# Optimization experiments

Measured on AMD Instinct MI355X. Metric: run time of the kernel, lower is better.

The kernel has to match this reference:

```python
import jax, jax.numpy as jnp
import numpy as np

NUM_HEADS = 16
WINDOW = 256  # window_size; tokens attend iff |i-j| <= WINDOW//2
LN_EPS = 1e-5


def setup_inputs() -> dict:
    key = jax.random.key(0)
    k1, k2, k3 = jax.random.split(key, 3)
    B, L, D = 2, 2048, 1024
    x = jax.random.normal(k1, (B, L, D), dtype=jnp.float32)
    w_qkv = jax.random.normal(k2, (3 * D, D), dtype=jnp.float32) * 0.02
    w_out = jax.random.normal(k3, (D, D), dtype=jnp.float32) * 0.02
    gamma = jnp.ones((D,), dtype=jnp.float32)
    beta = jnp.zeros((D,), dtype=jnp.float32)
    return {"x": x, "w_qkv": w_qkv, "w_out": w_out, "gamma": gamma, "beta": beta}


def reference(x, w_qkv, w_out, gamma, beta):
    B, L, D = x.shape
    H = NUM_HEADS
    HD = D // H
    residual = x
    # LayerNorm
    mu = jnp.mean(x, axis=-1, keepdims=True)
    var = jnp.mean(jnp.square(x - mu), axis=-1, keepdims=True)
    xn = (x - mu) * jax.lax.rsqrt(var + LN_EPS) * gamma + beta
    # QKV projection (torch Linear: y = x @ W.T)
    qkv = jnp.einsum('bld,ed->ble', xn, w_qkv).reshape(B, L, 3, H, HD)
    qkv = jnp.transpose(qkv, (2, 0, 3, 1, 4))  # [3, B, H, L, HD]
    q, k, v = qkv[0], qkv[1], qkv[2]
    # Dense scores with banded window mask (same math as the torch module)
    scores = jnp.einsum('bhqd,bhkd->bhqk', q, k) / jnp.sqrt(jnp.float32(HD))
    idx = jnp.arange(L)
    band = jnp.abs(idx[:, None] - idx[None, :]) <= (WINDOW // 2)  # [L, L] bool
    scores = jnp.where(band[None, None], scores, -jnp.inf)
    attn = jax.nn.softmax(scores, axis=-1)
    out = jnp.einsum('bhqk,bhkd->bhqd', attn, v)  # [B, H, L, HD]
    out = jnp.transpose(out, (0, 2, 1, 3)).reshape(B, L, D)
    return residual + jnp.einsum('bld,ed->ble', out, w_out)
```

## Files before the change

kernel.cpp:

```cpp
#include <hip/hip_runtime.h>

typedef unsigned int u32;
typedef unsigned short u16;
typedef __attribute__((ext_vector_type(8))) short short8;
typedef __attribute__((ext_vector_type(4))) float f32x4;

#define LSEQ 2048
#define DM 1024
#define HWIN 128

__device__ __forceinline__ u16 f2bf(float f) {
  union { float f; u32 u; } v; v.f = f;
  u32 r = v.u + 0x7FFFu + ((v.u >> 16) & 1u);
  return (u16)(r >> 16);
}
__device__ __forceinline__ u32 packbf(float lo, float hi) {
  return (u32)f2bf(lo) | ((u32)f2bf(hi) << 16);
}

typedef __attribute__((address_space(3))) u32 lds_u32;
typedef __attribute__((address_space(1))) const u32 glob_u32;
__device__ __forceinline__ void g2lds16(const void* g, void* l) {
  __builtin_amdgcn_global_load_lds((glob_u32*)g, (lds_u32*)l, 16, 0, 0);
}

__global__ __launch_bounds__(256) void ln_kernel(const float* __restrict__ x,
                                                 const float* __restrict__ gamma,
                                                 const float* __restrict__ beta,
                                                 u16* __restrict__ xn) {
  int r = blockIdx.x;
  int t = threadIdx.x;
  const float4* xr = (const float4*)(x + (size_t)r * DM);
  float4 v = xr[t];
  float s = v.x + v.y + v.z + v.w;
  float s2 = v.x * v.x + v.y * v.y + v.z * v.z + v.w * v.w;
#pragma unroll
  for (int o = 32; o; o >>= 1) { s += __shfl_xor(s, o); s2 += __shfl_xor(s2, o); }
  __shared__ float ws1[4], ws2[4];
  if ((t & 63) == 0) { ws1[t >> 6] = s; ws2[t >> 6] = s2; }
  __syncthreads();
  s = ws1[0] + ws1[1] + ws1[2] + ws1[3];
  s2 = ws2[0] + ws2[1] + ws2[2] + ws2[3];
  float mu = s * (1.0f / DM);
  float var = s2 * (1.0f / DM) - mu * mu;
  float rs = rsqrtf(var + 1e-5f);
  float4 g = ((const float4*)gamma)[t];
  float4 b = ((const float4*)beta)[t];
  u32 lo = packbf((v.x - mu) * rs * g.x + b.x, (v.y - mu) * rs * g.y + b.y);
  u32 hi = packbf((v.z - mu) * rs * g.z + b.z, (v.w - mu) * rs * g.w + b.w);
  u32* dst = (u32*)(xn + (size_t)r * DM) + t * 2;
  dst[0] = lo; dst[1] = hi;
}

__global__ __launch_bounds__(256) void cvt2_kernel(const float* __restrict__ a,
                                                   const float* __restrict__ b,
                                                   u16* __restrict__ oa,
                                                   u16* __restrict__ ob) {
  int blk = blockIdx.x;
  const float* in; u16* out; int i;
  if (blk < 3072) { in = a; out = oa; i = blk * 256 + threadIdx.x; }
  else            { in = b; out = ob; i = (blk - 3072) * 256 + threadIdx.x; }
  float4 v = ((const float4*)in)[i];
  u32* dst = (u32*)out + i * 2;
  dst[0] = packbf(v.x, v.y);
  dst[1] = packbf(v.z, v.w);
}

__device__ __forceinline__ void stage_tile(const u16* __restrict__ G, int gr0, int K,
                                           int k0, u16* lbuf, int tid, int w) {
#pragma unroll
  for (int j = 0; j < 4; ++j) {
    int rp = j * 32 + (tid >> 3);
    int ce = ((tid & 7) ^ (rp & 7)) * 8;
    g2lds16(G + (size_t)(gr0 + rp) * K + k0 + ce, lbuf + j * 2048 + w * 512);
  }
}

template <int MODE>
__global__ __launch_bounds__(256) void gemm_bt(const u16* __restrict__ Ag,
                                               const u16* __restrict__ Bg,
                                               int K, int NB,
                                               u16* __restrict__ qk_out,
                                               u16* __restrict__ vt_out,
                                               const float* __restrict__ resid,
                                               float* __restrict__ out) {
  __shared__ __align__(16) u16 sm[32768];
  int tid = threadIdx.x;
  int w = tid >> 6, l = tid & 63;
  int lg = l >> 4, li = l & 15;
  int bm = blockIdx.x / NB, bn = blockIdx.x % NB;
  int wr = w >> 1, wc = w & 1;
  f32x4 acc[4][4];
#pragma unroll
  for (int m = 0; m < 4; ++m)
#pragma unroll
    for (int n = 0; n < 4; ++n) acc[m][n] = (f32x4){0.f, 0.f, 0.f, 0.f};

  int nt = K >> 6;
  stage_tile(Ag, bm * 128, K, 0, sm, tid, w);
  stage_tile(Bg, bn * 128, K, 0, sm + 8192, tid, w);
  asm volatile("s_waitcnt vmcnt(0)" ::: "memory");
  __builtin_amdgcn_s_barrier();
  asm volatile("" ::: "memory");

  int cur = 0;
  for (int t = 0; t < nt; ++t) {
    if (t + 1 < nt) {
      stage_tile(Ag, bm * 128, K, (t + 1) << 6, sm + (cur ^ 1) * 16384, tid, w);
      stage_tile(Bg, bn * 128, K, (t + 1) << 6, sm + (cur ^ 1) * 16384 + 8192, tid, w);
    }
    const u16* Ab = sm + cur * 16384;
    const u16* Bb = Ab + 8192;
#pragma unroll
    for (int ks = 0; ks < 2; ++ks) {
      short8 af[4], bf4[4];
#pragma unroll
      for (int m = 0; m < 4; ++m)
        af[m] = *(const short8*)&Ab[(wr * 64 + m * 16 + li) * 64 + (((lg + ks * 4) ^ (li & 7)) * 8)];
#pragma unroll
      for (int n = 0; n < 4; ++n)
        bf4[n] = *(const short8*)&Bb[(wc * 64 + n * 16 + li) * 64 + (((lg + ks * 4) ^ (li & 7)) * 8)];
#pragma unroll
      for (int m = 0; m < 4; ++m)
#pragma unroll
        for (int n = 0; n < 4; ++n)
          acc[m][n] = __builtin_amdgcn_mfma_f32_16x16x32_bf16(af[m], bf4[n], acc[m][n], 0, 0, 0);
    }
    asm volatile("s_waitcnt vmcnt(0)" ::: "memory");
    __builtin_amdgcn_s_barrier();
    asm volatile("" ::: "memory");
    cur ^= 1;
  }

  int colbase = bn * 128 + wc * 64;
  int rowbase = bm * 128 + wr * 64;
#pragma unroll
  for (int m = 0; m < 4; ++m) {
    int row = rowbase + m * 16 + lg * 4;
#pragma unroll
    for (int n = 0; n < 4; ++n) {
      int col = colbase + n * 16 + li;
      if (MODE == 0) {
        if (colbase < 2048) {
#pragma unroll
          for (int r = 0; r < 4; ++r)
            qk_out[(size_t)(row + r) * 2048 + col] = f2bf(acc[m][n][r]);
        } else {
          int b = row >> 11;
          int hdcol = col - 2048;
          size_t idx = ((size_t)b * 1024 + hdcol) * 2048 + (row & 2047);
          u32* d = (u32*)&vt_out[idx];
          d[0] = packbf(acc[m][n][0], acc[m][n][1]);
          d[1] = packbf(acc[m][n][2], acc[m][n][3]);
        }
      } else {
#pragma unroll
        for (int r = 0; r < 4; ++r) {
          size_t idx = (size_t)(row + r) * 1024 + col;
          out[idx] = resid[idx] + acc[m][n][r];
        }
      }
    }
  }
}

__global__ __launch_bounds__(256) void attn_kernel(const u16* __restrict__ qk,
                                                   const u16* __restrict__ vt,
                                                   u16* __restrict__ ato) {
  int blk = blockIdx.x;
  int bh = blk >> 5;
  int qblk = blk & 31;
  int b = bh >> 4, h = bh & 15;
  int tid = threadIdx.x;
  int w = tid >> 6, l = tid & 63;
  int lg = l >> 4, li = l & 15;
  int qw = qblk * 64 + w * 16;
  int q = qw + li;

  const u16* qbase = qk + (size_t)(b * 2048 + q) * 2048 + h * 64 + lg * 8;
  short8 qf0 = *(const short8*)qbase;
  short8 qf1 = *(const short8*)(qbase + 32);

  const u16* kbase = qk + (size_t)b * 2048 * 2048 + 1024 + h * 64 + lg * 8;
  const u16* vbase = vt + (size_t)(bh * 64 + li) * 2048;

  f32x4 o0 = {0,0,0,0}, o1 = {0,0,0,0}, o2 = {0,0,0,0}, o3 = {0,0,0,0};
  float m = -1e30f, lsum = 0.f;

  int lo = qw - HWIN; if (lo < 0) lo = 0;
  int hi = qw + 15 + HWIN; if (hi > LSEQ - 1) hi = LSEQ - 1;
  const float SC = 0.125f * 1.44269504088896f;

  for (int kb = lo & ~31; kb <= hi; kb += 32) {
    const u16* kp0 = kbase + (size_t)(kb + li) * 2048;
    const u16* kp1 = kbase + (size_t)(kb + 16 + li) * 2048;
    short8 k00 = *(const short8*)kp0;
    short8 k01 = *(const short8*)(kp0 + 32);
    short8 k10 = *(const short8*)kp1;
    short8 k11 = *(const short8*)(kp1 + 32);
    f32x4 c0 = {0,0,0,0}, c1 = {0,0,0,0};
    c0 = __builtin_amdgcn_mfma_f32_16x16x32_bf16(k00, qf0, c0, 0, 0, 0);
    c0 = __builtin_amdgcn_mfma_f32_16x16x32_bf16(k01, qf1, c0, 0, 0, 0);
    c1 = __builtin_amdgcn_mfma_f32_16x16x32_bf16(k10, qf0, c1, 0, 0, 0);
    c1 = __builtin_amdgcn_mfma_f32_16x16x32_bf16(k11, qf1, c1, 0, 0, 0);

    float t[8];
    bool interior = (kb >= qw + 15 - HWIN) && (kb + 31 <= qw + HWIN) && (kb + 31 < LSEQ);
    if (interior) {
#pragma unroll
      for (int r = 0; r < 4; ++r) { t[r] = c0[r] * SC; t[r + 4] = c1[r] * SC; }
    } else {
#pragma unroll
      for (int r = 0; r < 4; ++r) {
        int key0 = kb + lg * 4 + r;
        int key1 = key0 + 16;
        int d0 = key0 - q, d1 = key1 - q;
        t[r]     = (d0 >= -HWIN && d0 <= HWIN && key0 < LSEQ) ? c0[r] * SC : -__builtin_inff();
        t[r + 4] = (d1 >= -HWIN && d1 <= HWIN && key1 < LSEQ) ? c1[r] * SC : -__builtin_inff();
      }
    }
    float mc = t[0];
#pragma unroll
    for (int i = 1; i < 8; ++i) mc = fmaxf(mc, t[i]);
    mc = fmaxf(mc, __shfl_xor(mc, 16));
    mc = fmaxf(mc, __shfl_xor(mc, 32));

    float p[8]; float ssum;
    if (__all(mc <= m + 8.0f)) {
      ssum = 0.f;
#pragma unroll
      for (int i = 0; i < 8; ++i) { p[i] = __builtin_amdgcn_exp2f(t[i] - m); ssum += p[i]; }
      ssum += __shfl_xor(ssum, 16);
      ssum += __shfl_xor(ssum, 32);
      lsum += ssum;
    } else {
      float mn = fmaxf(m, mc);
      float corr = __builtin_amdgcn_exp2f(m - mn);
      ssum = 0.f;
#pragma unroll
      for (int i = 0; i < 8; ++i) { p[i] = __builtin_amdgcn_exp2f(t[i] - mn); ssum += p[i]; }
      ssum += __shfl_xor(ssum, 16);
      ssum += __shfl_xor(ssum, 32);
      lsum = lsum * corr + ssum;
      m = mn;
      o0 *= corr; o1 *= corr; o2 *= corr; o3 *= corr;
    }

    u32 a0 = packbf(p[0], p[1]);
    u32 a1 = packbf(p[2], p[3]);
    u32 b0 = packbf(p[4], p[5]);
    u32 b1 = packbf(p[6], p[7]);
    int sg0 = (((2 * lg) & 3) << 4) + li;
    int sg1 = (((2 * lg + 1) & 3) << 4) + li;
    u32 w0 = (u32)__shfl((int)a0, sg0), w1 = (u32)__shfl((int)a1, sg0);
    u32 w2 = (u32)__shfl((int)a0, sg1), w3 = (u32)__shfl((int)a1, sg1);
    u32 x0 = (u32)__shfl((int)b0, sg0), x1 = (u32)__shfl((int)b1, sg0);
    u32 x2 = (u32)__shfl((int)b0, sg1), x3 = (u32)__shfl((int)b1, sg1);
    bool lohalf = lg < 2;
    union { u32 u[4]; short8 s; } pf;
    pf.u[0] = lohalf ? w0 : x0;
    pf.u[1] = lohalf ? w1 : x1;
    pf.u[2] = lohalf ? w2 : x2;
    pf.u[3] = lohalf ? w3 : x3;

    const u16* vp = vbase + kb + lg * 8;
    short8 v0 = *(const short8*)(vp);
    short8 v1 = *(const short8*)(vp + (size_t)16 * 2048);
    short8 v2 = *(const short8*)(vp + (size_t)32 * 2048);
    short8 v3 = *(const short8*)(vp + (size_t)48 * 2048);
    o0 = __builtin_amdgcn_mfma_f32_16x16x32_bf16(v0, pf.s, o0, 0, 0, 0);
    o1 = __builtin_amdgcn_mfma_f32_16x16x32_bf16(v1, pf.s, o1, 0, 0, 0);
    o2 = __builtin_amdgcn_mfma_f32_16x16x32_bf16(v2, pf.s, o2, 0, 0, 0);
    o3 = __builtin_amdgcn_mfma_f32_16x16x32_bf16(v3, pf.s, o3, 0, 0, 0);
  }

  float inv = 1.0f / lsum;
  u16* orow = ato + (size_t)(b * 2048 + q) * 1024 + h * 64 + lg * 4;
  *(u32*)(orow +  0) = packbf(o0[0] * inv, o0[1] * inv);
  *(u32*)(orow +  2) = packbf(o0[2] * inv, o0[3] * inv);
  *(u32*)(orow + 16) = packbf(o1[0] * inv, o1[1] * inv);
  *(u32*)(orow + 18) = packbf(o1[2] * inv, o1[3] * inv);
  *(u32*)(orow + 32) = packbf(o2[0] * inv, o2[1] * inv);
  *(u32*)(orow + 34) = packbf(o2[2] * inv, o2[3] * inv);
  *(u32*)(orow + 48) = packbf(o3[0] * inv, o3[1] * inv);
  *(u32*)(orow + 50) = packbf(o3[2] * inv, o3[3] * inv);
}

extern "C" void kernel_launch(void* const* d_in, const int* in_sizes, int n_in,
                              void* d_out, int out_size, void* d_ws, size_t ws_size,
                              hipStream_t stream) {
  const float* x     = (const float*)d_in[0];
  const float* w_qkv = (const float*)d_in[1];
  const float* w_out = (const float*)d_in[2];
  const float* gamma = (const float*)d_in[3];
  const float* beta  = (const float*)d_in[4];
  float* out = (float*)d_out;
  char* ws = (char*)d_ws;

  u16* xn  = (u16*)(ws);
  u16* wq  = (u16*)(ws + 8388608);
  u16* wo  = (u16*)(ws + 14680064);
  u16* qkb = (u16*)(ws + 16777216);
  u16* vt  = (u16*)(ws + 33554432);
  u16* ao  = (u16*)(ws + 41943040);

  ln_kernel<<<4096, 256, 0, stream>>>(x, gamma, beta, xn);
  cvt2_kernel<<<4096, 256, 0, stream>>>(w_qkv, w_out, wq, wo);
  gemm_bt<0><<<32 * 24, 256, 0, stream>>>(xn, wq, 1024, 24, qkb, vt, nullptr, nullptr);
  attn_kernel<<<32 * 32, 256, 0, stream>>>(qkb, vt, ao);
  gemm_bt<1><<<32 * 8, 256, 0, stream>>>(ao, wo, 1024, 8, nullptr, nullptr, x, out);
}
```

Baseline: 105.8 us.

## Software-pipeline K/V loads in attention and merge LN with weight conversion

The attention loop now double-buffers K and V register fragments, issuing the next chunk's global loads before computing the current one. The per-chunk cross-lane row-sum reduction is deferred to a single reduction after the loop, and the redundant sequence-end checks are dropped. Launch bounds request 4 blocks per SM. Separately, the LayerNorm and weight bf16 conversion kernels are merged into one launch to cut one kernel launch. The double-buffered fragments raise register pressure, which may reduce occupancy.

```diff
diff --git a/kernel.cpp b/kernel.cpp
--- a/kernel.cpp
+++ b/kernel.cpp
@@ -24,12 +24,27 @@
   __builtin_amdgcn_global_load_lds((glob_u32*)g, (lds_u32*)l, 16, 0, 0);
 }
 
-__global__ __launch_bounds__(256) void ln_kernel(const float* __restrict__ x,
-                                                 const float* __restrict__ gamma,
-                                                 const float* __restrict__ beta,
-                                                 u16* __restrict__ xn) {
-  int r = blockIdx.x;
+__global__ __launch_bounds__(256) void ln_cvt_kernel(const float* __restrict__ x,
+                                                     const float* __restrict__ gamma,
+                                                     const float* __restrict__ beta,
+                                                     u16* __restrict__ xn,
+                                                     const float* __restrict__ wqi,
+                                                     const float* __restrict__ woi,
+                                                     u16* __restrict__ wq,
+                                                     u16* __restrict__ wo) {
+  int blk = blockIdx.x;
   int t = threadIdx.x;
+  if (blk >= 4096) {
+    const float* in; u16* out; int i;
+    if (blk < 7168) { in = wqi; out = wq; i = (blk - 4096) * 256 + t; }
+    else            { in = woi; out = wo; i = (blk - 7168) * 256 + t; }
+    float4 v = ((const float4*)in)[i];
+    u32* dst = (u32*)out + i * 2;
+    dst[0] = packbf(v.x, v.y);
+    dst[1] = packbf(v.z, v.w);
+    return;
+  }
+  int r = blk;
   const float4* xr = (const float4*)(x + (size_t)r * DM);
   float4 v = xr[t];
   float s = v.x + v.y + v.z + v.w;
@@ -52,20 +67,6 @@
   dst[0] = lo; dst[1] = hi;
 }
 
-__global__ __launch_bounds__(256) void cvt2_kernel(const float* __restrict__ a,
-                                                   const float* __restrict__ b,
-                                                   u16* __restrict__ oa,
-                                                   u16* __restrict__ ob) {
-  int blk = blockIdx.x;
-  const float* in; u16* out; int i;
-  if (blk < 3072) { in = a; out = oa; i = blk * 256 + threadIdx.x; }
-  else            { in = b; out = ob; i = (blk - 3072) * 256 + threadIdx.x; }
-  float4 v = ((const float4*)in)[i];
-  u32* dst = (u32*)out + i * 2;
-  dst[0] = packbf(v.x, v.y);
-  dst[1] = packbf(v.z, v.w);
-}
-
 __device__ __forceinline__ void stage_tile(const u16* __restrict__ G, int gr0, int K,
                                            int k0, u16* lbuf, int tid, int w) {
 #pragma unroll
@@ -164,9 +165,100 @@
   }
 }
 
-__global__ __launch_bounds__(256) void attn_kernel(const u16* __restrict__ qk,
-                                                   const u16* __restrict__ vt,
-                                                   u16* __restrict__ ato) {
+__device__ __forceinline__ void process_chunk(
+    short8 k00, short8 k01, short8 k10, short8 k11,
+    short8 v0, short8 v1, short8 v2, short8 v3,
+    short8 qf0, short8 qf1,
+    int kb, int qw, int q, int lg, int sg0, int sg1,
+    float& mrun, float& lsum, f32x4& o0, f32x4& o1, f32x4& o2, f32x4& o3) {
+  const float SC = 0.125f * 1.44269504088896f;
+  f32x4 c0 = {0,0,0,0}, c1 = {0,0,0,0};
+  c0 = __builtin_amdgcn_mfma_f32_16x16x32_bf16(k00, qf0, c0, 0, 0, 0);
+  c0 = __builtin_amdgcn_mfma_f32_16x16x32_bf16(k01, qf1, c0, 0, 0, 0);
+  c1 = __builtin_amdgcn_mfma_f32_16x16x32_bf16(k10, qf0, c1, 0, 0, 0);
+  c1 = __builtin_amdgcn_mfma_f32_16x16x32_bf16(k11, qf1, c1, 0, 0, 0);
+
+  float t[8];
+  bool interior = (kb >= qw + 15 - HWIN) && (kb + 31 <= qw + HWIN);
+  if (interior) {
+#pragma unroll
+    for (int r = 0; r < 4; ++r) { t[r] = c0[r] * SC; t[r + 4] = c1[r] * SC; }
+  } else {
+#pragma unroll
+    for (int r = 0; r < 4; ++r) {
+      int key0 = kb + lg * 4 + r;
+      int key1 = key0 + 16;
+      int d0 = key0 - q, d1 = key1 - q;
+      t[r]     = (d0 >= -HWIN && d0 <= HWIN) ? c0[r] * SC : -__builtin_inff();
+      t[r + 4] = (d1 >= -HWIN && d1 <= HWIN) ? c1[r] * SC : -__builtin_inff();
+    }
+  }
+  float mA = fmaxf(fmaxf(t[0], t[1]), fmaxf(t[2], t[3]));
+  float mB = fmaxf(fmaxf(t[4], t[5]), fmaxf(t[6], t[7]));
+  float mc = fmaxf(mA, mB);
+  mc = fmaxf(mc, __shfl_xor(mc, 16));
+  mc = fmaxf(mc, __shfl_xor(mc, 32));
+
+  float p[8];
+  if (__all(mc <= mrun + 8.0f)) {
+    float s0 = 0.f;
+#pragma unroll
+    for (int i = 0; i < 8; ++i) { p[i] = __builtin_amdgcn_exp2f(t[i] - mrun); s0 += p[i]; }
+    lsum += s0;
+  } else {
+    float mn = fmaxf(mrun, mc);
+    float corr = __builtin_amdgcn_exp2f(mrun - mn);
+    float s0 = 0.f;
+#pragma unroll
+    for (int i = 0; i < 8; ++i) { p[i] = __builtin_amdgcn_exp2f(t[i] - mn); s0 += p[i]; }
+    lsum = lsum * corr + s0;
+    mrun = mn;
+    o0 *= corr; o1 *= corr; o2 *= corr; o3 *= corr;
+  }
+
+  u32 a0 = packbf(p[0], p[1]);
+  u32 a1 = packbf(p[2], p[3]);
+  u32 b0 = packbf(p[4], p[5]);
+  u32 b1 = packbf(p[6], p[7]);
+  u32 w0 = (u32)__shfl((int)a0, sg0), w1 = (u32)__shfl((int)a1, sg0);
+  u32 w2 = (u32)__shfl((int)a0, sg1), w3 = (u32)__shfl((int)a1, sg1);
+  u32 x0 = (u32)__shfl((int)b0, sg0), x1 = (u32)__shfl((int)b1, sg0);
+  u32 x2 = (u32)__shfl((int)b0, sg1), x3 = (u32)__shfl((int)b1, sg1);
+  bool lohalf = lg < 2;
+  union { u32 u[4]; short8 s; } pf;
+  pf.u[0] = lohalf ? w0 : x0;
+  pf.u[1] = lohalf ? w1 : x1;
+  pf.u[2] = lohalf ? w2 : x2;
+  pf.u[3] = lohalf ? w3 : x3;
+
+  o0 = __builtin_amdgcn_mfma_f32_16x16x32_bf16(v0, pf.s, o0, 0, 0, 0);
+  o1 = __builtin_amdgcn_mfma_f32_16x16x32_bf16(v1, pf.s, o1, 0, 0, 0);
+  o2 = __builtin_amdgcn_mfma_f32_16x16x32_bf16(v2, pf.s, o2, 0, 0, 0);
+  o3 = __builtin_amdgcn_mfma_f32_16x16x32_bf16(v3, pf.s, o3, 0, 0, 0);
+}
+
+#define LOADKV(P, kb)                                                        \
+  do {                                                                       \
+    const u16* kp0_ = kbase + (size_t)((kb) + li) * 2048;                    \
+    const u16* kp1_ = kp0_ + (size_t)16 * 2048;                              \
+    P##k00 = *(const short8*)kp0_;                                           \
+    P##k01 = *(const short8*)(kp0_ + 32);                                    \
+    P##k10 = *(const short8*)kp1_;                                           \
+    P##k11 = *(const short8*)(kp1_ + 32);                                    \
+    const u16* vp_ = vbase + (kb) + lg * 8;                                  \
+    P##v0 = *(const short8*)vp_;                                             \
+    P##v1 = *(const short8*)(vp_ + (size_t)16 * 2048);                       \
+    P##v2 = *(const short8*)(vp_ + (size_t)32 * 2048);                       \
+    P##v3 = *(const short8*)(vp_ + (size_t)48 * 2048);                       \
+  } while (0)
+
+#define PROC(P, kb)                                                          \
+  process_chunk(P##k00, P##k01, P##k10, P##k11, P##v0, P##v1, P##v2, P##v3,  \
+                qf0, qf1, (kb), qw, q, lg, sg0, sg1, mrun, lsum, o0, o1, o2, o3)
+
+__global__ __launch_bounds__(256, 4) void attn_kernel(const u16* __restrict__ qk,
+                                                      const u16* __restrict__ vt,
+                                                      u16* __restrict__ ato) {
   int blk = blockIdx.x;
   int bh = blk >> 5;
   int qblk = blk & 31;
@@ -176,6 +268,8 @@
   int lg = l >> 4, li = l & 15;
   int qw = qblk * 64 + w * 16;
   int q = qw + li;
+  int sg0 = (((2 * lg) & 3) << 4) + li;
+  int sg1 = (((2 * lg + 1) & 3) << 4) + li;
 
   const u16* qbase = qk + (size_t)(b * 2048 + q) * 2048 + h * 64 + lg * 8;
   short8 qf0 = *(const short8*)qbase;
@@ -185,95 +279,29 @@
   const u16* vbase = vt + (size_t)(bh * 64 + li) * 2048;
 
   f32x4 o0 = {0,0,0,0}, o1 = {0,0,0,0}, o2 = {0,0,0,0}, o3 = {0,0,0,0};
-  float m = -1e30f, lsum = 0.f;
+  float mrun = -1e30f, lsum = 0.f;
 
   int lo = qw - HWIN; if (lo < 0) lo = 0;
   int hi = qw + 15 + HWIN; if (hi > LSEQ - 1) hi = LSEQ - 1;
-  const float SC = 0.125f * 1.44269504088896f;
-
-  for (int kb = lo & ~31; kb <= hi; kb += 32) {
-    const u16* kp0 = kbase + (size_t)(kb + li) * 2048;
-    const u16* kp1 = kbase + (size_t)(kb + 16 + li) * 2048;
-    short8 k00 = *(const short8*)kp0;
-    short8 k01 = *(const short8*)(kp0 + 32);
-    short8 k10 = *(const short8*)kp1;
-    short8 k11 = *(const short8*)(kp1 + 32);
-    f32x4 c0 = {0,0,0,0}, c1 = {0,0,0,0};
-    c0 = __builtin_amdgcn_mfma_f32_16x16x32_bf16(k00, qf0, c0, 0, 0, 0);
-    c0 = __builtin_amdgcn_mfma_f32_16x16x32_bf16(k01, qf1, c0, 0, 0, 0);
-    c1 = __builtin_amdgcn_mfma_f32_16x16x32_bf16(k10, qf0, c1, 0, 0, 0);
-    c1 = __builtin_amdgcn_mfma_f32_16x16x32_bf16(k11, qf1, c1, 0, 0, 0);
-
-    float t[8];
-    bool interior = (kb >= qw + 15 - HWIN) && (kb + 31 <= qw + HWIN) && (kb + 31 < LSEQ);
-    if (interior) {
-#pragma unroll
-      for (int r = 0; r < 4; ++r) { t[r] = c0[r] * SC; t[r + 4] = c1[r] * SC; }
-    } else {
-#pragma unroll
-      for (int r = 0; r < 4; ++r) {
-        int key0 = kb + lg * 4 + r;
-        int key1 = key0 + 16;
-        int d0 = key0 - q, d1 = key1 - q;
-        t[r]     = (d0 >= -HWIN && d0 <= HWIN && key0 < LSEQ) ? c0[r] * SC : -__builtin_inff();
-        t[r + 4] = (d1 >= -HWIN && d1 <= HWIN && key1 < LSEQ) ? c1[r] * SC : -__builtin_inff();
-      }
-    }
-    float mc = t[0];
-#pragma unroll
-    for (int i = 1; i < 8; ++i) mc = fmaxf(mc, t[i]);
-    mc = fmaxf(mc, __shfl_xor(mc, 16));
-    mc = fmaxf(mc, __shfl_xor(mc, 32));
-
-    float p[8]; float ssum;
-    if (__all(mc <= m + 8.0f)) {
-      ssum = 0.f;
-#pragma unroll
-      for (int i = 0; i < 8; ++i) { p[i] = __builtin_amdgcn_exp2f(t[i] - m); ssum += p[i]; }
-      ssum += __shfl_xor(ssum, 16);
-      ssum += __shfl_xor(ssum, 32);
-      lsum += ssum;
-    } else {
-      float mn = fmaxf(m, mc);
-      float corr = __builtin_amdgcn_exp2f(m - mn);
-      ssum = 0.f;
-#pragma unroll
-      for (int i = 0; i < 8; ++i) { p[i] = __builtin_amdgcn_exp2f(t[i] - mn); ssum += p[i]; }
-      ssum += __shfl_xor(ssum, 16);
-      ssum += __shfl_xor(ssum, 32);
-      lsum = lsum * corr + ssum;
-      m = mn;
-      o0 *= corr; o1 *= corr; o2 *= corr; o3 *= corr;
-    }
-
-    u32 a0 = packbf(p[0], p[1]);
-    u32 a1 = packbf(p[2], p[3]);
-    u32 b0 = packbf(p[4], p[5]);
-    u32 b1 = packbf(p[6], p[7]);
-    int sg0 = (((2 * lg) & 3) << 4) + li;
-    int sg1 = (((2 * lg + 1) & 3) << 4) + li;
-    u32 w0 = (u32)__shfl((int)a0, sg0), w1 = (u32)__shfl((int)a1, sg0);
-    u32 w2 = (u32)__shfl((int)a0, sg1), w3 = (u32)__shfl((int)a1, sg1);
-    u32 x0 = (u32)__shfl((int)b0, sg0), x1 = (u32)__shfl((int)b1, sg0);
-    u32 x2 = (u32)__shfl((int)b0, sg1), x3 = (u32)__shfl((int)b1, sg1);
-    bool lohalf = lg < 2;
-    union { u32 u[4]; short8 s; } pf;
-    pf.u[0] = lohalf ? w0 : x0;
-    pf.u[1] = lohalf ? w1 : x1;
-    pf.u[2] = lohalf ? w2 : x2;
-    pf.u[3] = lohalf ? w3 : x3;
-
-    const u16* vp = vbase + kb + lg * 8;
-    short8 v0 = *(const short8*)(vp);
-    short8 v1 = *(const short8*)(vp + (size_t)16 * 2048);
-    short8 v2 = *(const short8*)(vp + (size_t)32 * 2048);
-    short8 v3 = *(const short8*)(vp + (size_t)48 * 2048);
-    o0 = __builtin_amdgcn_mfma_f32_16x16x32_bf16(v0, pf.s, o0, 0, 0, 0);
-    o1 = __builtin_amdgcn_mfma_f32_16x16x32_bf16(v1, pf.s, o1, 0, 0, 0);
-    o2 = __builtin_amdgcn_mfma_f32_16x16x32_bf16(v2, pf.s, o2, 0, 0, 0);
-    o3 = __builtin_amdgcn_mfma_f32_16x16x32_bf16(v3, pf.s, o3, 0, 0, 0);
-  }
-
+  int kb0 = lo & ~31;
+  int n = ((hi - kb0) >> 5) + 1;
+
+  short8 Ak00, Ak01, Ak10, Ak11, Av0, Av1, Av2, Av3;
+  short8 Bk00, Bk01, Bk10, Bk11, Bv0, Bv1, Bv2, Bv3;
+
+  LOADKV(A, kb0);
+  int c = 0;
+  for (; c + 2 <= n; c += 2) {
+    int kb = kb0 + (c << 5);
+    LOADKV(B, kb + 32);
+    PROC(A, kb);
+    if (c + 2 < n) LOADKV(A, kb + 64);
+    PROC(B, kb + 32);
+  }
+  if (c < n) PROC(A, kb0 + (c << 5));
+
+  lsum += __shfl_xor(lsum, 16);
+  lsum += __shfl_xor(lsum, 32);
   float inv = 1.0f / lsum;
   u16* orow = ato + (size_t)(b * 2048 + q) * 1024 + h * 64 + lg * 4;
   *(u32*)(orow +  0) = packbf(o0[0] * inv, o0[1] * inv);
@@ -304,8 +332,7 @@
   u16* vt  = (u16*)(ws + 33554432);
   u16* ao  = (u16*)(ws + 41943040);
 
-  ln_kernel<<<4096, 256, 0, stream>>>(x, gamma, beta, xn);
-  cvt2_kernel<<<4096, 256, 0, stream>>>(w_qkv, w_out, wq, wo);
+  ln_cvt_kernel<<<8192, 256, 0, stream>>>(x, gamma, beta, xn, w_qkv, w_out, wq, wo);
   gemm_bt<0><<<32 * 24, 256, 0, stream>>>(xn, wq, 1024, 24, qkb, vt, nullptr, nullptr);
   attn_kernel<<<32 * 32, 256, 0, stream>>>(qkb, vt, ao);
   gemm_bt<1><<<32 * 8, 256, 0, stream>>>(ao, wo, 1024, 8, nullptr, nullptr, x, out);
```

Measured after the change: 138.9 us. 31.3% more time.
